# Kernel tuning notes

Hardware: AMD Instinct MI355X
Metric: run time of the kernel (lower is better)

The kernel has to match this reference:

```python
import jax, jax.numpy as jnp
import numpy as np

B, N, K, C, DK, DV, H, W = 16, 5, 5, 512, 128, 128, 16, 16

def setup_inputs() -> dict:
    key = jax.random.key(0)
    k1, k2, k3, k4 = jax.random.split(key, 4)
    return {
        "query_repr": jax.random.normal(k1, (B, C, H, W), dtype=jnp.float32),
        "supports_repr": jax.random.normal(k2, (B, N, K, C, H, W), dtype=jnp.float32),
        "w_qk": jax.random.normal(k3, (DK, C), dtype=jnp.float32) * (C ** -0.5),
        "w_v": jax.random.normal(k4, (DV, C), dtype=jnp.float32) * (C ** -0.5),
    }

def reference(query_repr, supports_repr, w_qk, w_v):
    scale = DK ** -0.5
    # 1x1 convs == per-pixel linear projections
    query_q = jnp.einsum('oc,bchw->bohw', w_qk, query_repr)          # [b,dk,h,w]
    query_v = jnp.einsum('oc,bchw->bohw', w_v, query_repr)           # [b,dv,h,w]
    supports_k = jnp.einsum('oc,bnkchw->bnkohw', w_qk, supports_repr)  # [b,n,k,dk,h,w]
    supports_v = jnp.einsum('oc,bnkchw->bnkohw', w_v, supports_repr)   # [b,n,k,dv,h,w]

    # attention: query pixel (h,w) attends over all support pixels (k,i,j)
    sim = jnp.einsum('bchw,bnkcij->bnhwkij', query_q, supports_k) * scale
    b, n, h, w = sim.shape[:4]
    attn = jax.nn.softmax(sim.reshape(b, n, h, w, -1), axis=-1)
    attn = attn.reshape(b, n, h, w, K, h, w)
    out = jnp.einsum('bnhwkij,bnkcij->bnchw', attn, supports_v)      # [b,n,dv,h,w]

    out = out.reshape(b, n, -1)                                      # [b,n,dv*h*w]
    qv = query_v.reshape(b, 1, -1)                                   # [b,1,dv*h*w]
    euclidean_dist = jnp.sum((qv - out) ** 2, axis=-1) / (h * w)     # [b,n]
    return -euclidean_dist
```

## Files before the change

kernel.cpp:

```cpp
#include <hip/hip_runtime.h>
#include <hip/hip_bf16.h>
#include <stdint.h>

constexpr int Bv = 16, Nv = 5, Kv = 5, Cv = 512, DKv = 128, DVv = 128, HWv = 256;
constexpr int NSUP = Bv * Nv * Kv;
constexpr int NSLAB = NSUP + Bv;

typedef __attribute__((ext_vector_type(8))) short bf16x8;
typedef __attribute__((ext_vector_type(4))) float f32x4;

static __device__ __forceinline__ unsigned short f2b(float x) {
  __hip_bfloat16 h = __float2bfloat16(x);
  return *reinterpret_cast<unsigned short*>(&h);
}

__global__ __launch_bounds__(256) void prep_kernel(
    const float* __restrict__ query, const float* __restrict__ w_qk,
    const float* __restrict__ w_v, unsigned short* __restrict__ WbF,
    unsigned short* __restrict__ Xb, float* __restrict__ out, int out_n) {
  __shared__ unsigned short lds[64][68];
  const int bid = blockIdx.x;
  const int tid = threadIdx.x;
  if (bid < 64) {
    int gidx = bid * 256 + tid;
    int l = gidx & 63;
    int nb = (gidx >> 6) & 7;
    int ks = (gidx >> 9) & 1;
    int kt = (gidx >> 10) & 7;
    int h = (gidx >> 13) & 1;
    int row = nb * 16 + (l & 15);
    int c0 = kt * 64 + ks * 32 + (l >> 4) * 8;
    const float* src = (h ? w_v : w_qk) + (size_t)row * Cv + c0;
    float4 a = *(const float4*)src;
    float4 b = *(const float4*)(src + 4);
    union { unsigned short u[8]; uint4 v; } t;
    t.u[0] = f2b(a.x); t.u[1] = f2b(a.y); t.u[2] = f2b(a.z); t.u[3] = f2b(a.w);
    t.u[4] = f2b(b.x); t.u[5] = f2b(b.y); t.u[6] = f2b(b.z); t.u[7] = f2b(b.w);
    *(uint4*)(WbF + (size_t)gidx * 8) = t.v;
  } else if (bid < 576) {
    const int blk = bid - 64;
    const int s = NSUP + (blk >> 5);
    const int tq = blk & 31;
    const int cb = tq >> 2, pb = tq & 3;
    const int c0 = cb * 64, p0 = pb * 64;
    const float* __restrict__ X = query + (size_t)(s - NSUP) * Cv * HWv;
#pragma unroll
    for (int r = 0; r < 4; ++r) {
      int cl = (tid >> 4) + r * 16;
      int pl = (tid & 15) * 4;
      float4 v = *(const float4*)(X + (size_t)(c0 + cl) * HWv + p0 + pl);
      ushort4 u;
      u.x = f2b(v.x); u.y = f2b(v.y); u.z = f2b(v.z); u.w = f2b(v.w);
      *(ushort4*)&lds[cl][pl] = u;
    }
    __syncthreads();
    const int pl2 = tid >> 2;
    const int q0 = (tid & 3) * 16;
    union { unsigned short u[16]; uint4 v4[2]; } tmp;
#pragma unroll
    for (int jj = 0; jj < 16; ++jj) {
      int j = (jj + pl2) & 15;
      tmp.u[j] = lds[q0 + j][pl2];
    }
    unsigned short* dst = Xb + ((size_t)s * HWv + p0 + pl2) * Cv + c0 + q0;
    *(uint4*)dst = tmp.v4[0];
    *((uint4*)dst + 1) = tmp.v4[1];
  } else {
    if (tid < out_n) out[tid] = 0.0f;
  }
}

__global__ __launch_bounds__(256, 2) void proj_all_kernel(
    const float* __restrict__ supports, const unsigned short* __restrict__ WbF,
    unsigned short* __restrict__ KbF, unsigned short* __restrict__ VbF,
    const unsigned short* __restrict__ Xb, unsigned short* __restrict__ Qb,
    float* __restrict__ QVf) {
  __shared__ __align__(16) char smem[24576];
  const int bid = blockIdx.x;
  const int t = threadIdx.x;
  const int lane = t & 63, wid = t >> 6;
  const int wr = wid >> 1, wc = wid & 1;
  const int l15 = lane & 15, g = lane >> 4;

  f32x4 acc[2][8] = {};

  if (bid < 1600) {
    const int s = bid >> 2;
    const int pixq = bid & 3;
    float* lds_f = (float*)smem;
    unsigned short* Xt = (unsigned short*)(smem + 16384);
    const float* __restrict__ Xs = supports + (size_t)s * Cv * HWv + pixq * 64;

    auto dma = [&](int kt) {
#pragma unroll
      for (int i = 0; i < 4; ++i) {
        const int seg = wid * 4 + i;
        const float* gsrc =
            Xs + (size_t)(kt * 64 + seg * 4 + (lane >> 4)) * HWv + (lane & 15) * 4;
        __builtin_amdgcn_global_load_lds(
            (const __attribute__((address_space(1))) void*)gsrc,
            (__attribute__((address_space(3))) void*)((char*)lds_f + seg * 1024),
            16, 0, 0);
      }
    };
    auto stageB = [&]() {
#pragma unroll
      for (int h2 = 0; h2 < 2; ++h2) {
        const int sidx = h2 * 256 + t;
        const int sslot = sidx >> 6;
        const int row = sidx & 63;
        union { unsigned short u[8]; uint4 q; } pk;
#pragma unroll
        for (int j = 0; j < 8; ++j)
          pk.u[j] = f2b(lds_f[(size_t)(sslot * 8 + j) * 64 + row]);
        *(uint4*)((char*)Xt + row * 128 + ((sslot ^ (row & 7)) * 16)) = pk.q;
      }
    };

    dma(0);
    __syncthreads();
    stageB();
    __syncthreads();
    for (int kt = 0; kt < 8; ++kt) {
      if (kt < 7) dma(kt + 1);
#pragma unroll
      for (int ks = 0; ks < 2; ++ks) {
        const int sx = ((ks * 4 + g) ^ (l15 & 7)) * 16;
        bf16x8 A[2], Bf[8];
#pragma unroll
        for (int m = 0; m < 2; ++m)
          A[m] = *(const bf16x8*)((const char*)Xt + (wr * 32 + m * 16 + l15) * 128 + sx);
#pragma unroll
        for (int n = 0; n < 8; ++n) {
          const int h = n >> 2;
          const int nb = wc * 4 + (n & 3);
          Bf[n] = *(const bf16x8*)(
              WbF + (size_t)((((h * 8 + kt) * 2 + ks) * 8 + nb) * 64 + lane) * 8);
        }
#pragma unroll
        for (int m = 0; m < 2; ++m)
#pragma unroll
          for (int n = 0; n < 8; ++n)
            acc[m][n] = __builtin_amdgcn_mfma_f32_16x16x32_bf16(A[m], Bf[n],
                                                                acc[m][n], 0, 0, 0);
      }
      __syncthreads();
      if (kt < 7) { stageB(); __syncthreads(); }
    }

    unsigned short* bounce = (unsigned short*)smem;
#pragma unroll
    for (int m = 0; m < 2; ++m) {
      const int pr = wr * 32 + m * 16 + g * 4;
#pragma unroll
      for (int n = 0; n < 4; ++n) {
        const int dk = wc * 64 + n * 16 + l15;
#pragma unroll
        for (int r = 0; r < 4; ++r)
          bounce[(size_t)(pr + r) * 140 + dk] = f2b(acc[m][n][r]);
      }
    }
    __syncthreads();
    {
      unsigned short* Kdst = KbF + ((size_t)s * 4 + pixq) * 8192;
#pragma unroll
      for (int i = 0; i < 4; ++i) {
        const int u = i * 256 + t;
        const int jl15 = u & 15, jg = (u >> 4) & 3, jkc = (u >> 6) & 3,
                  jnc = (u >> 8) & 3;
        const int pixl = jnc * 16 + jl15;
        const int dk = jkc * 32 + jg * 8;
        *(uint4*)(Kdst + (size_t)u * 8) = *(const uint4*)(bounce + (size_t)pixl * 140 + dk);
      }
    }
    __syncthreads();
#pragma unroll
    for (int m = 0; m < 2; ++m) {
      const int pr = wr * 32 + m * 16 + g * 4;
#pragma unroll
      for (int n = 0; n < 4; ++n) {
        const int dv = wc * 64 + n * 16 + l15;
#pragma unroll
        for (int r = 0; r < 4; ++r)
          bounce[(size_t)dv * 72 + pr + r] = f2b(acc[m][4 + n][r]);
      }
    }
    __syncthreads();
    {
      unsigned short* Vdst = VbF + ((size_t)s * 4 + pixq) * 8192;
#pragma unroll
      for (int i = 0; i < 4; ++i) {
        const int u = i * 256 + t;
        const int jl15 = u & 15, jg = (u >> 4) & 3, jd = (u >> 6) & 7,
                  jkc2 = (u >> 9) & 1;
        const int dv = jd * 16 + jl15;
        const int nsl = jkc2 * 32 + jg * 8;
        *(uint4*)(Vdst + (size_t)u * 8) = *(const uint4*)(bounce + (size_t)dv * 72 + nsl);
      }
    }
  } else {
    const int r0 = bid - 1600;
    const int sq = r0 >> 2;
    const int pixq = r0 & 3;
    unsigned short* Xt2 = (unsigned short*)smem;
    const unsigned short* __restrict__ Xq =
        Xb + ((size_t)(NSUP + sq) * HWv + pixq * 64) * Cv;

    auto dmaQ = [&](int kt, int buf) {
#pragma unroll
      for (int i = 0; i < 2; ++i) {
        const int seg = wid * 2 + i;
        const int row = seg * 8 + (lane >> 3);
        const int srcslot = (lane & 7) ^ ((lane >> 3) & 7);
        const unsigned short* gsrc = Xq + (size_t)row * Cv + kt * 64 + srcslot * 8;
        __builtin_amdgcn_global_load_lds(
            (const __attribute__((address_space(1))) void*)gsrc,
            (__attribute__((address_space(3))) void*)((char*)Xt2 + buf * 8192 + seg * 1024),
            16, 0, 0);
      }
    };

    dmaQ(0, 0);
    __syncthreads();
    for (int kt = 0; kt < 8; ++kt) {
      const int cur = kt & 1;
      if (kt < 7) dmaQ(kt + 1, cur ^ 1);
      const char* Xt = (const char*)Xt2 + cur * 8192;
#pragma unroll
      for (int ks = 0; ks < 2; ++ks) {
        const int sx = ((ks * 4 + g) ^ (l15 & 7)) * 16;
        bf16x8 A[2], Bf[8];
#pragma unroll
        for (int m = 0; m < 2; ++m)
          A[m] = *(const bf16x8*)(Xt + (wr * 32 + m * 16 + l15) * 128 + sx);
#pragma unroll
        for (int n = 0; n < 8; ++n) {
          const int h = n >> 2;
          const int nb = wc * 4 + (n & 3);
          Bf[n] = *(const bf16x8*)(
              WbF + (size_t)((((h * 8 + kt) * 2 + ks) * 8 + nb) * 64 + lane) * 8);
        }
#pragma unroll
        for (int m = 0; m < 2; ++m)
#pragma unroll
          for (int n = 0; n < 8; ++n)
            acc[m][n] = __builtin_amdgcn_mfma_f32_16x16x32_bf16(A[m], Bf[n],
                                                                acc[m][n], 0, 0, 0);
      }
      __syncthreads();
    }

#pragma unroll
    for (int m = 0; m < 2; ++m) {
      const int pixr = pixq * 64 + wr * 32 + m * 16 + g * 4;
#pragma unroll
      for (int n = 0; n < 4; ++n) {
        const int oc = wc * 64 + n * 16 + l15;
        unsigned short* p = Qb + ((size_t)sq * HWv + pixr) * DKv + oc;
#pragma unroll
        for (int r = 0; r < 4; ++r) p[(size_t)r * DKv] = f2b(acc[m][n][r]);
      }
#pragma unroll
      for (int n = 0; n < 4; ++n) {
        const int oc = wc * 64 + n * 16 + l15;
        float* p = QVf + ((size_t)sq * HWv + pixr) * DVv + oc;
#pragma unroll
        for (int r = 0; r < 4; ++r) p[(size_t)r * DVv] = acc[m][4 + n][r];
      }
    }
  }
}

__global__ __launch_bounds__(256) void attn_mfma_kernel(
    const unsigned short* __restrict__ KbF, const unsigned short* __restrict__ VbF,
    const unsigned short* __restrict__ Qb, const float* __restrict__ QVf,
    float* __restrict__ out) {
  __shared__ __align__(16) char smem[74784];
  unsigned short* Klds = (unsigned short*)smem;
  unsigned short* Vlds = (unsigned short*)(smem + 32768);
  unsigned short* Plds = (unsigned short*)(smem + 65536);
  float* redbuf = (float*)(smem + 74752);

  const int L = blockIdx.x;
  const int bid = (L & 7) * 40 + (L >> 3);
  const int bn = bid >> 2, qh = bid & 3;
  const int b = bn / Nv;
  const int t = threadIdx.x;
  const int l = t & 63, wid = t >> 6;
  const int l15 = l & 15, g = l >> 4;
  const int qpix0 = qh * 64 + wid * 16;
  constexpr float C2 = 0.08838834764831845f * 1.4426950408889634f;

  bf16x8 qa[4];
#pragma unroll
  for (int kc = 0; kc < 4; ++kc)
    qa[kc] = *(const bf16x8*)(
        Qb + ((size_t)(b * HWv + qpix0 + l15)) * DKv + kc * 32 + g * 8);

  f32x4 oacc[8] = {};
  float mrow[4], lrow[4];
#pragma unroll
  for (int r = 0; r < 4; ++r) { mrow[r] = -3e38f; lrow[r] = 0.0f; }

  unsigned short* Pw = Plds + wid * 16 * 72;

  auto dma = [&](int c, int buf) {
    const int s2 = bn * Kv + (c >> 2);
    const int chunk = c & 3;
    const unsigned short* Kc = KbF + ((size_t)s2 * 4 + chunk) * 8192;
    const unsigned short* Vc = VbF + ((size_t)s2 * 4 + chunk) * 8192;
#pragma unroll
    for (int i = 0; i < 4; ++i) {
      const int seg = wid * 4 + i;
      __builtin_amdgcn_global_load_lds(
          (const __attribute__((address_space(1))) void*)(Kc + (size_t)(seg * 64 + l) * 8),
          (__attribute__((address_space(3))) void*)(Klds + (size_t)buf * 8192 + seg * 512),
          16, 0, 0);
      __builtin_amdgcn_global_load_lds(
          (const __attribute__((address_space(1))) void*)(Vc + (size_t)(seg * 64 + l) * 8),
          (__attribute__((address_space(3))) void*)(Vlds + (size_t)buf * 8192 + seg * 512),
          16, 0, 0);
    }
  };

  dma(0, 0);
  __syncthreads();
  for (int c = 0; c < 20; ++c) {
    const int cur = c & 1;
    if (c < 19) dma(c + 1, cur ^ 1);
    const unsigned short* Kc = Klds + (size_t)cur * 8192;
    const unsigned short* Vc = Vlds + (size_t)cur * 8192;

    f32x4 s4[4];
#pragma unroll
    for (int nc = 0; nc < 4; ++nc) {
      f32x4 sv = {};
#pragma unroll
      for (int kc = 0; kc < 4; ++kc) {
        bf16x8 kf = *(const bf16x8*)(Kc + (size_t)((nc * 4 + kc) * 64 + l) * 8);
        sv = __builtin_amdgcn_mfma_f32_16x16x32_bf16(qa[kc], kf, sv, 0, 0, 0);
      }
      s4[nc] = sv;
    }
    float pm[4];
#pragma unroll
    for (int r = 0; r < 4; ++r) {
      float v = s4[0][r];
#pragma unroll
      for (int nc = 1; nc < 4; ++nc) v = fmaxf(v, s4[nc][r]);
      pm[r] = v;
    }
#pragma unroll
    for (int off = 1; off <= 8; off <<= 1)
#pragma unroll
      for (int r = 0; r < 4; ++r) pm[r] = fmaxf(pm[r], __shfl_xor(pm[r], off));
    float sc[4];
#pragma unroll
    for (int r = 0; r < 4; ++r) {
      float mn = fmaxf(mrow[r], pm[r]);
      sc[r] = exp2f(C2 * (mrow[r] - mn));
      mrow[r] = mn;
      lrow[r] *= sc[r];
    }
#pragma unroll
    for (int d = 0; d < 8; ++d)
#pragma unroll
      for (int r = 0; r < 4; ++r) oacc[d][r] *= sc[r];
#pragma unroll
    for (int nc = 0; nc < 4; ++nc)
#pragma unroll
      for (int r = 0; r < 4; ++r) {
        float p = exp2f(C2 * (s4[nc][r] - mrow[r]));
        lrow[r] += p;
        Pw[(size_t)(g * 4 + r) * 72 + nc * 16 + l15] = f2b(p);
      }
#pragma unroll
    for (int kc2 = 0; kc2 < 2; ++kc2) {
      bf16x8 pa = *(const bf16x8*)(Pw + (size_t)l15 * 72 + kc2 * 32 + g * 8);
#pragma unroll
      for (int d = 0; d < 8; ++d) {
        bf16x8 vf = *(const bf16x8*)(Vc + (size_t)((kc2 * 8 + d) * 64 + l) * 8);
        oacc[d] = __builtin_amdgcn_mfma_f32_16x16x32_bf16(pa, vf, oacc[d], 0, 0, 0);
      }
    }
    __syncthreads();
  }

#pragma unroll
  for (int off = 1; off <= 8; off <<= 1)
#pragma unroll
    for (int r = 0; r < 4; ++r) lrow[r] += __shfl_xor(lrow[r], off);
  float linv[4];
#pragma unroll
  for (int r = 0; r < 4; ++r) linv[r] = 1.0f / lrow[r];

  float part = 0.0f;
#pragma unroll
  for (int d = 0; d < 8; ++d)
#pragma unroll
    for (int r = 0; r < 4; ++r) {
      float o = oacc[d][r] * linv[r];
      float qv = QVf[((size_t)(b * HWv + qpix0 + g * 4 + r)) * DVv + d * 16 + l15];
      float df = qv - o;
      part += df * df;
    }
#pragma unroll
  for (int off = 1; off <= 32; off <<= 1) part += __shfl_xor(part, off);
  if (l == 0) redbuf[wid] = part;
  __syncthreads();
  if (t == 0) {
    float tot = redbuf[0] + redbuf[1] + redbuf[2] + redbuf[3];
    atomicAdd(out + bn, -tot * (1.0f / HWv));
  }
}

extern "C" void kernel_launch(void* const* d_in, const int* in_sizes, int n_in,
                              void* d_out, int out_size, void* d_ws, size_t ws_size,
                              hipStream_t stream) {
  const float* query = (const float*)d_in[0];
  const float* supports = (const float*)d_in[1];
  const float* w_qk = (const float*)d_in[2];
  const float* w_v = (const float*)d_in[3];
  float* out = (float*)d_out;

  const size_t sz_kb = (size_t)NSUP * 4 * 8192 * 2;
  const size_t sz_vb = (size_t)NSUP * 4 * 8192 * 2;
  const size_t sz_qb = (size_t)Bv * HWv * DKv * 2;
  const size_t sz_qvf = (size_t)Bv * HWv * DVv * 4;
  const size_t sz_xb = (size_t)NSLAB * HWv * Cv * 2;
  const size_t sz_wb = (size_t)256 * Cv * 2;

  char* p = (char*)d_ws;
  unsigned short* KbF = (unsigned short*)p;           p += sz_kb;
  unsigned short* VbF = (unsigned short*)p;           p += sz_vb;
  unsigned short* Qb = (unsigned short*)p;            p += sz_qb;
  float* QVf = (float*)p;                             p += sz_qvf;
  unsigned short* Xb = (unsigned short*)p;            p += sz_xb;
  p += sz_wb;
  unsigned short* WbF = (unsigned short*)p;

  prep_kernel<<<577, 256, 0, stream>>>(query, w_qk, w_v, WbF, Xb, out, out_size);
  proj_all_kernel<<<1664, 256, 0, stream>>>(supports, WbF, KbF, VbF, Xb, Qb, QVf);
  attn_mfma_kernel<<<Bv * Nv * 4, 256, 0, stream>>>(KbF, VbF, Qb, QVf, out);
}
```

Measured before the change: 154.2 us.

## Deepen projection prefetch pipeline with double-buffered staging and explicit waitcnt barriers

The support-projection path now double-buffers both the fp32 DMA staging area and the bf16 transposed tile, prefetching two K-tiles ahead instead of one. The query path moves from two to four LDS buffers, also prefetching two ahead. Full __syncthreads are replaced by explicit vmcnt/lgkmcnt waits around raw s_barrier calls, with sched_barrier fences between them. LDS grows to 48KB and the occupancy hint rises from 2 to 3 blocks, trading LDS capacity for more latency hiding. This depends on the hand-tuned wait counts matching the loads actually outstanding.

```diff
diff --git a/kernel.cpp b/kernel.cpp
--- a/kernel.cpp
+++ b/kernel.cpp
@@ -13,6 +13,11 @@
   __hip_bfloat16 h = __float2bfloat16(x);
   return *reinterpret_cast<unsigned short*>(&h);
 }
+
+#define SB0() __builtin_amdgcn_sched_barrier(0)
+#define BARRIER() __builtin_amdgcn_s_barrier()
+#define WAITVM(N) asm volatile("s_waitcnt vmcnt(" #N ")" ::: "memory")
+#define WAITLGKM0() asm volatile("s_waitcnt lgkmcnt(0)" ::: "memory")
 
 __global__ __launch_bounds__(256) void prep_kernel(
     const float* __restrict__ query, const float* __restrict__ w_qk,
@@ -70,12 +75,12 @@
   }
 }
 
-__global__ __launch_bounds__(256, 2) void proj_all_kernel(
+__global__ __launch_bounds__(256, 3) void proj_all_kernel(
     const float* __restrict__ supports, const unsigned short* __restrict__ WbF,
     unsigned short* __restrict__ KbF, unsigned short* __restrict__ VbF,
     const unsigned short* __restrict__ Xb, unsigned short* __restrict__ Qb,
     float* __restrict__ QVf) {
-  __shared__ __align__(16) char smem[24576];
+  __shared__ __align__(16) char smem[49152];
   const int bid = blockIdx.x;
   const int t = threadIdx.x;
   const int lane = t & 63, wid = t >> 6;
@@ -87,11 +92,13 @@
   if (bid < 1600) {
     const int s = bid >> 2;
     const int pixq = bid & 3;
-    float* lds_f = (float*)smem;
-    unsigned short* Xt = (unsigned short*)(smem + 16384);
+    float* F0 = (float*)smem;
+    float* F1 = (float*)(smem + 16384);
+    unsigned short* X0 = (unsigned short*)(smem + 32768);
+    unsigned short* X1 = (unsigned short*)(smem + 40960);
     const float* __restrict__ Xs = supports + (size_t)s * Cv * HWv + pixq * 64;
 
-    auto dma = [&](int kt) {
+    auto dma = [&](int kt, float* dstF) {
 #pragma unroll
       for (int i = 0; i < 4; ++i) {
         const int seg = wid * 4 + i;
@@ -99,11 +106,11 @@
             Xs + (size_t)(kt * 64 + seg * 4 + (lane >> 4)) * HWv + (lane & 15) * 4;
         __builtin_amdgcn_global_load_lds(
             (const __attribute__((address_space(1))) void*)gsrc,
-            (__attribute__((address_space(3))) void*)((char*)lds_f + seg * 1024),
+            (__attribute__((address_space(3))) void*)((char*)dstF + seg * 1024),
             16, 0, 0);
       }
     };
-    auto stageB = [&]() {
+    auto stageB = [&](const float* srcF, unsigned short* dstX) {
 #pragma unroll
       for (int h2 = 0; h2 < 2; ++h2) {
         const int sidx = h2 * 256 + t;
@@ -112,24 +119,29 @@
         union { unsigned short u[8]; uint4 q; } pk;
 #pragma unroll
         for (int j = 0; j < 8; ++j)
-          pk.u[j] = f2b(lds_f[(size_t)(sslot * 8 + j) * 64 + row]);
-        *(uint4*)((char*)Xt + row * 128 + ((sslot ^ (row & 7)) * 16)) = pk.q;
+          pk.u[j] = f2b(srcF[(size_t)(sslot * 8 + j) * 64 + row]);
+        *(uint4*)((char*)dstX + row * 128 + ((sslot ^ (row & 7)) * 16)) = pk.q;
       }
     };
 
-    dma(0);
-    __syncthreads();
-    stageB();
-    __syncthreads();
+    dma(0, F0);
+    dma(1, F1);
+    SB0(); WAITVM(4); SB0(); BARRIER(); SB0();
+    stageB(F0, X0);
+    WAITLGKM0(); SB0(); BARRIER(); SB0();
+
     for (int kt = 0; kt < 8; ++kt) {
-      if (kt < 7) dma(kt + 1);
+      const int cur = kt & 1;
+      float* Fc = cur ? F1 : F0;
+      const unsigned short* Xc = cur ? X1 : X0;
+      if (kt < 6) dma(kt + 2, Fc);
 #pragma unroll
       for (int ks = 0; ks < 2; ++ks) {
         const int sx = ((ks * 4 + g) ^ (l15 & 7)) * 16;
         bf16x8 A[2], Bf[8];
 #pragma unroll
         for (int m = 0; m < 2; ++m)
-          A[m] = *(const bf16x8*)((const char*)Xt + (wr * 32 + m * 16 + l15) * 128 + sx);
+          A[m] = *(const bf16x8*)((const char*)Xc + (wr * 32 + m * 16 + l15) * 128 + sx);
 #pragma unroll
         for (int n = 0; n < 8; ++n) {
           const int h = n >> 2;
@@ -144,8 +156,15 @@
             acc[m][n] = __builtin_amdgcn_mfma_f32_16x16x32_bf16(A[m], Bf[n],
                                                                 acc[m][n], 0, 0, 0);
       }
-      __syncthreads();
-      if (kt < 7) { stageB(); __syncthreads(); }
+      if (kt < 7) {
+        SB0();
+        if (kt < 6) { WAITVM(4); } else { WAITVM(0); }
+        SB0(); BARRIER(); SB0();
+        float* Fn = cur ? F0 : F1;
+        unsigned short* Xn = cur ? X0 : X1;
+        stageB(Fn, Xn);
+        WAITLGKM0(); SB0(); BARRIER(); SB0();
+      }
     }
 
     unsigned short* bounce = (unsigned short*)smem;
@@ -221,11 +240,11 @@
     };
 
     dmaQ(0, 0);
-    __syncthreads();
+    dmaQ(1, 1);
+    SB0(); WAITVM(2); SB0(); BARRIER(); SB0();
     for (int kt = 0; kt < 8; ++kt) {
-      const int cur = kt & 1;
-      if (kt < 7) dmaQ(kt + 1, cur ^ 1);
-      const char* Xt = (const char*)Xt2 + cur * 8192;
+      if (kt < 6) dmaQ(kt + 2, (kt + 2) & 3);
+      const char* Xt = (const char*)Xt2 + (kt & 3) * 8192;
 #pragma unroll
       for (int ks = 0; ks < 2; ++ks) {
         const int sx = ((ks * 4 + g) ^ (l15 & 7)) * 16;
@@ -247,7 +266,11 @@
             acc[m][n] = __builtin_amdgcn_mfma_f32_16x16x32_bf16(A[m], Bf[n],
                                                                 acc[m][n], 0, 0, 0);
       }
-      __syncthreads();
+      if (kt < 7) {
+        SB0();
+        if (kt < 6) { WAITVM(2); } else { WAITVM(0); }
+        SB0(); BARRIER(); SB0();
+      }
     }
 
 #pragma unroll
```

Result: no change. 152.8 us (-0.9%).
